# Optimization experiments

Measured on AMD Instinct MI355X. Metric: run time of the kernel, lower is better.

The kernel has to match this reference:

```python
import jax, jax.numpy as jnp
import numpy as np

B, Z, H, T = 256, 512, 1024, 512   # batch, z_size, hidden (conductor==decoder), num_tokens
L, N = 16, 16                      # num_levels, notes_per_bar


def setup_inputs() -> dict:
    key = jax.random.key(0)
    ks = jax.random.split(key, 16)
    s = 0.05  # weight init scale
    rn = lambda k, shp, sc=1.0: sc * jax.random.normal(k, shp, dtype=jnp.float32)
    return {
        "z": rn(ks[0], (B, L * N, 1, Z)),
        "dec_h0": rn(ks[1], (L, B, H)),
        "dec_c0": rn(ks[2], (L, B, H)),
        # linear_in (computed but unused by the original forward)
        "lin_in_W": rn(ks[3], (Z, Z), s), "lin_in_b": rn(ks[4], (Z,), s),
        # conductor LSTM (input Z -> hidden H), PyTorch gate order i,f,g,o
        "cond_Wih": rn(ks[5], (4 * H, Z), s), "cond_Whh": rn(ks[6], (4 * H, H), s),
        "cond_bih": rn(ks[7], (4 * H,), s), "cond_bhh": rn(ks[8], (4 * H,), s),
        # decoder LSTM (input T+H -> hidden H)
        "dec_Wih": rn(ks[9], (4 * H, T + H), s), "dec_Whh": rn(ks[10], (4 * H, H), s),
        "dec_bih": rn(ks[11], (4 * H,), s), "dec_bhh": rn(ks[12], (4 * H,), s),
        # output projection
        "out_W": rn(ks[13], (T, H), s), "out_b": rn(ks[14], (T,), s),
    }


def _lstm_cell(x, h, c, Wih, Whh, b):
    gates = x @ Wih.T + h @ Whh.T + b            # [B, 4H]
    i, f, g, o = jnp.split(gates, 4, axis=-1)
    c = jax.nn.sigmoid(f) * c + jax.nn.sigmoid(i) * jnp.tanh(g)
    h = jax.nn.sigmoid(o) * jnp.tanh(c)
    return h, c


def reference(z, dec_h0, dec_c0, lin_in_W, lin_in_b,
              cond_Wih, cond_Whh, cond_bih, cond_bhh,
              dec_Wih, dec_Whh, dec_bih, dec_bhh, out_W, out_b):
    Bsz = z.shape[0]
    Tt = out_b.shape[0]
    Hh = cond_Whh.shape[1]

    _unused = z @ lin_in_W.T + lin_in_b  # linear_in output is discarded in the source

    cond_b = cond_bih + cond_bhh
    dec_b = dec_bih + dec_bhh

    # conductor consumes z[:, L*level, 0, :] for each level
    z_lv = jnp.transpose(z[:, jnp.arange(L) * L, 0, :], (1, 0, 2))  # [L, B, Z]

    def level_step(carry, xs):
        ch, cc = carry
        zl, dh, dc = xs
        ch, cc = _lstm_cell(zl, ch, cc, cond_Wih, cond_Whh, cond_b)
        emb = ch  # [B, H], fixed conductor embedding for this bar

        def note_step(c2, _):
            note, dh2, dc2 = c2
            inp = jnp.concatenate([emb, note], axis=-1)  # [B, H+T]
            dh2, dc2 = _lstm_cell(inp, dh2, dc2, dec_Wih, dec_Whh, dec_b)
            out = jax.nn.sigmoid(dh2 @ out_W.T + out_b)  # [B, T]
            return (out, dh2, dc2), out

        note0 = jnp.zeros((Bsz, Tt), dtype=z.dtype)
        _, outs = jax.lax.scan(note_step, (note0, dh, dc), None, length=N)  # [N, B, T]
        return (ch, cc), outs

    h0 = jnp.zeros((Bsz, Hh), dtype=z.dtype)
    _, all_outs = jax.lax.scan(level_step, (h0, h0), (z_lv, dec_h0, dec_c0))  # [L, N, B, T]
    notes = jnp.transpose(all_outs, (2, 0, 1, 3)).reshape(Bsz, L * N, Tt)
    return notes
```

## Files before the change

kernel.cpp:

```cpp
#include <hip/hip_runtime.h>

typedef __bf16 bf16;
typedef __attribute__((ext_vector_type(8))) __bf16 bf16x8;
typedef __attribute__((ext_vector_type(4))) float f32x4;
typedef __attribute__((ext_vector_type(4))) unsigned short u16x4;

__device__ __forceinline__ void gload_lds16(const void* g, void* l) {
  __builtin_amdgcn_global_load_lds(
      (const __attribute__((address_space(1))) void*)g,
      (__attribute__((address_space(3))) void*)l, 16, 0, 0);
}

__device__ __forceinline__ float sigmoidf_(float x) { return 1.0f / (1.0f + expf(-x)); }

__device__ __forceinline__ float bf2f(unsigned short u) {
  union { unsigned int i; float f; } v;
  v.i = ((unsigned int)u) << 16;
  return v.f;
}
__device__ __forceinline__ unsigned short f2bfbits(float x) {
  union { bf16 b; unsigned short u; } v;
  v.b = (bf16)x;
  return v.u;
}

#define SB() __builtin_amdgcn_sched_barrier(0)
#define MFMA16(a, b, c) __builtin_amdgcn_mfma_f32_16x16x32_bf16(a, b, c, 0, 0, 0)

template<int MODE>
__global__ __launch_bounds__(512, 2)
void gemm8(const bf16* __restrict__ A, int lda,
           const bf16* __restrict__ Bw, int K,
           bf16* __restrict__ Cb,
           const bf16* __restrict__ X, const float* __restrict__ bias,
           bf16* __restrict__ cst, bf16* __restrict__ hout, int ldh) {
  extern __shared__ __align__(16) char smem_raw[];
  bf16* lsA = (bf16*)smem_raw;
  bf16* lsB = lsA + 4 * 8192;

  const int tid = threadIdx.x;
  const int lane = tid & 63;
  const int wave = tid >> 6;
  const int wm = wave >> 2, wn = wave & 3;

  const int bid = blockIdx.x;
  const int k8 = bid & 7;
  const int l = bid >> 3;
  const int mt = (k8 & 1) * 8 + (l & 7);
  const int nt = (k8 >> 1) * 4 + (l >> 3);
  const int m0 = mt * 256, n0 = nt * 256;

  const int nkt = K >> 5;

  const int srow = tid >> 2;
  const int scol = ((tid & 3) ^ ((srow >> 1) & 3)) * 8;
  const bf16* gAs = A + (size_t)(m0 + srow) * lda + scol;
  const bf16* gBs = Bw + (size_t)(n0 + srow) * K + scol;

  auto stA = [&](int kt) {
    bf16* d = lsA + (kt & 3) * 8192 + tid * 8;
    const bf16* s = gAs + (size_t)kt * 32;
    gload_lds16(s, d);
    gload_lds16(s + (size_t)128 * lda, d + 4096);
  };
  auto stB = [&](int kt) {
    bf16* d = lsB + (kt & 3) * 8192 + tid * 8;
    const bf16* s = gBs + (size_t)kt * 32;
    gload_lds16(s, d);
    gload_lds16(s + (size_t)128 * K, d + 4096);
  };

  const int sw = ((lane & 15) >> 1) & 3;
  const int rslot = ((lane >> 4) ^ sw) * 8;
  const int abase = (wm * 128 + (lane & 15)) * 32 + rslot;
  const int bbase = (wn * 64 + (lane & 15)) * 32 + rslot;

  f32x4 acc[8][4] = {};

  stA(0); stB(0); stA(1); stB(1);
  asm volatile("s_waitcnt vmcnt(4)" ::: "memory");

  for (int t = 0; t < nkt; ++t) {
    SB();
    __builtin_amdgcn_s_barrier();
    SB();
    const bf16* pA = lsA + (t & 3) * 8192;
    const bf16* pB = lsB + (t & 3) * 8192;
    bf16x8 av[8], bv[4];
#pragma unroll
    for (int f = 0; f < 8; ++f) av[f] = *(const bf16x8*)&pA[abase + f * 512];
#pragma unroll
    for (int g = 0; g < 4; ++g) bv[g] = *(const bf16x8*)&pB[bbase + g * 512];
    if (t + 2 < nkt) { stA(t + 2); stB(t + 2); }
    asm volatile("s_waitcnt lgkmcnt(0)" ::: "memory");
    SB();
    __builtin_amdgcn_s_setprio(1);
#pragma unroll
    for (int f = 0; f < 8; ++f)
#pragma unroll
      for (int g = 0; g < 4; ++g)
        acc[f][g] = MFMA16(av[f], bv[g], acc[f][g]);
    __builtin_amdgcn_s_setprio(0);
    if (t + 2 < nkt)      asm volatile("s_waitcnt vmcnt(4)" ::: "memory");
    else if (t + 1 < nkt) asm volatile("s_waitcnt vmcnt(0)" ::: "memory");
  }

  const int jj = lane & 15;
  const int rb = m0 + wm * 128 + ((lane >> 4) << 2);
  const int q = (n0 >> 6) + wn;
  if constexpr (MODE == 0) {
#pragma unroll
    for (int f = 0; f < 8; ++f)
#pragma unroll
      for (int r = 0; r < 4; ++r) {
        u16x4 pk;
        pk[0] = f2bfbits(acc[f][0][r]);
        pk[1] = f2bfbits(acc[f][1][r]);
        pk[2] = f2bfbits(acc[f][2][r]);
        pk[3] = f2bfbits(acc[f][3][r]);
        *(u16x4*)&Cb[(size_t)(rb + f * 16 + r) * 4096 + q * 64 + jj * 4] = pk;
      }
  } else {
    const int j = q * 16 + jj;
    const f32x4 bq = *(const f32x4*)&bias[q * 64 + jj * 4];
#pragma unroll
    for (int f = 0; f < 8; ++f) {
#pragma unroll
      for (int r = 0; r < 4; ++r) {
        const int row = rb + f * 16 + r;
        const u16x4 xv = __builtin_nontemporal_load(
            (const u16x4*)&X[(size_t)row * 4096 + q * 64 + jj * 4]);
        const float gi = acc[f][0][r] + bf2f(xv[0]) + bq[0];
        const float gf = acc[f][1][r] + bf2f(xv[1]) + bq[1];
        const float gg = acc[f][2][r] + bf2f(xv[2]) + bq[2];
        const float go = acc[f][3][r] + bf2f(xv[3]) + bq[3];
        const size_t ci = (size_t)row * 1024 + j;
        const float cold = bf2f(((const unsigned short*)cst)[ci]);
        const float cn = sigmoidf_(gf) * cold + sigmoidf_(gi) * tanhf(gg);
        cst[ci] = (bf16)cn;
        hout[(size_t)row * ldh + j] = (bf16)(sigmoidf_(go) * tanhf(cn));
      }
    }
  }
}

template<int BM, int BN, int WM, int WN, int MODE>
__global__ __launch_bounds__(WM * WN * 64)
void gemm_bt(const bf16* __restrict__ A, int lda,
             const bf16* __restrict__ Bw, int ldb,
             float* __restrict__ C, int ldc, int K,
             const float* __restrict__ outb, float* __restrict__ dout,
             bf16* __restrict__ anote, int nstep) {
  constexpr int BK = 64;
  constexpr int THREADS = WM * WN * 64;
  constexpr int SM = BM / WM, SN = BN / WN;
  constexpr int FM = SM / 16, FN = SN / 16;

  __shared__ __align__(16) bf16 lsA[BM * BK];
  __shared__ __align__(16) bf16 lsB[BN * BK];

  const int tid = threadIdx.x;
  const int lane = tid & 63;
  const int wave = tid >> 6;
  const int wm = wave / WN, wn = wave % WN;

  int mi = blockIdx.y, ni = blockIdx.x;
  if constexpr (MODE == 1) {
    const int flat = blockIdx.y * 8 + blockIdx.x;
    mi = (flat & 7) * 4 + ((flat >> 3) & 3);
    ni = flat >> 5;
  }
  const int m0 = mi * BM;
  const int n0 = ni * BN;

  f32x4 acc[FM][FN] = {};

  const bf16* gA = A + (size_t)m0 * lda;
  const bf16* gB = Bw + (size_t)n0 * ldb;

  for (int k0 = 0; k0 < K; k0 += BK) {
#pragma unroll
    for (int i = 0; i < (BM * 8) / THREADS; ++i) {
      int idx = i * THREADS + tid;
      gload_lds16(gA + (size_t)(idx >> 3) * lda + k0 + (idx & 7) * 8, &lsA[idx * 8]);
    }
#pragma unroll
    for (int i = 0; i < (BN * 8) / THREADS; ++i) {
      int idx = i * THREADS + tid;
      gload_lds16(gB + (size_t)(idx >> 3) * ldb + k0 + (idx & 7) * 8, &lsB[idx * 8]);
    }
    __syncthreads();

#pragma unroll
    for (int kk = 0; kk < BK; kk += 32) {
      bf16x8 av[FM], bv[FN];
#pragma unroll
      for (int i = 0; i < FM; ++i)
        av[i] = *(const bf16x8*)&lsA[(wm * SM + i * 16 + (lane & 15)) * BK + kk + (lane >> 4) * 8];
#pragma unroll
      for (int j = 0; j < FN; ++j)
        bv[j] = *(const bf16x8*)&lsB[(wn * SN + j * 16 + (lane & 15)) * BK + kk + (lane >> 4) * 8];
#pragma unroll
      for (int i = 0; i < FM; ++i)
#pragma unroll
        for (int j = 0; j < FN; ++j)
          acc[i][j] = MFMA16(av[i], bv[j], acc[i][j]);
    }
    __syncthreads();
  }

#pragma unroll
  for (int i = 0; i < FM; ++i) {
#pragma unroll
    for (int j = 0; j < FN; ++j) {
      const int col = n0 + wn * SN + j * 16 + (lane & 15);
      const int rbase = m0 + wm * SM + i * 16 + ((lane >> 4) << 2);
#pragma unroll
      for (int r = 0; r < 4; ++r) {
        const int row = rbase + r;
        float v = acc[i][j][r];
        if constexpr (MODE == 0) {
          C[(size_t)row * ldc + col] = v;
        } else {
          v = sigmoidf_(v + outb[col]);
          const int l = row >> 8, b = row & 255;
          dout[((size_t)(b * 256 + l * 16 + nstep)) * 512 + col] = v;
          anote[(size_t)row * 1536 + col] = (bf16)v;
        }
      }
    }
  }
}

template<int BM, int BJ, int WM, int WJ>
__global__ __launch_bounds__(WM * WJ * 64, 2)
void gemm_cell(const bf16* __restrict__ A, int lda,
               const bf16* __restrict__ Bw,
               const bf16* __restrict__ X,
               const float* __restrict__ bias,
               float* __restrict__ cst,
               bf16* __restrict__ hout, int ldh, int K) {
  constexpr int BK = 64;
  constexpr int THREADS = WM * WJ * 64;
  constexpr int BN = BJ * 64;
  constexpr int SM = BM / WM;
  constexpr int TJ = BJ / WJ;
  constexpr int FM = SM / 16;

  __shared__ __align__(16) bf16 lsA[BM * BK];
  __shared__ __align__(16) bf16 lsB[BN * BK];

  const int tid = threadIdx.x;
  const int lane = tid & 63;
  const int wave = tid >> 6;
  const int wm = wave / WJ, wj = wave % WJ;

  int qbi = blockIdx.x, mi = blockIdx.y;
  if constexpr (BM == 32 && BJ == 2) {
    const int flat = blockIdx.y * 32 + blockIdx.x;
    qbi = (flat & 7) * 4 + ((flat >> 3) & 3);
    mi = flat >> 5;
  }
  const int m0 = mi * BM;
  const int qb = qbi * BJ;

  f32x4 acc[FM][TJ][4] = {};

  const bf16* gA = A + (size_t)m0 * lda;
  const bf16* gB = Bw + (size_t)(qb * 64) * K;

  for (int k0 = 0; k0 < K; k0 += BK) {
#pragma unroll
    for (int i = 0; i < (BM * 8) / THREADS; ++i) {
      int idx = i * THREADS + tid;
      gload_lds16(gA + (size_t)(idx >> 3) * lda + k0 + (idx & 7) * 8, &lsA[idx * 8]);
    }
#pragma unroll
    for (int i = 0; i < (BN * 8) / THREADS; ++i) {
      int idx = i * THREADS + tid;
      gload_lds16(gB + (size_t)(idx >> 3) * K + k0 + (idx & 7) * 8, &lsB[idx * 8]);
    }
    __syncthreads();

#pragma unroll
    for (int kk = 0; kk < BK; kk += 32) {
      bf16x8 av[FM], bv[TJ][4];
#pragma unroll
      for (int i = 0; i < FM; ++i)
        av[i] = *(const bf16x8*)&lsA[(wm * SM + i * 16 + (lane & 15)) * BK + kk + (lane >> 4) * 8];
#pragma unroll
      for (int t = 0; t < TJ; ++t)
#pragma unroll
        for (int g = 0; g < 4; ++g)
          bv[t][g] = *(const bf16x8*)
              &lsB[((wj * TJ + t) * 64 + g * 16 + (lane & 15)) * BK + kk + (lane >> 4) * 8];
#pragma unroll
      for (int i = 0; i < FM; ++i)
#pragma unroll
        for (int t = 0; t < TJ; ++t)
#pragma unroll
          for (int g = 0; g < 4; ++g)
            acc[i][t][g] = MFMA16(av[i], bv[t][g], acc[i][t][g]);
    }
    __syncthreads();
  }

#pragma unroll
  for (int i = 0; i < FM; ++i) {
#pragma unroll
    for (int t = 0; t < TJ; ++t) {
      const int q = qb + wj * TJ + t;
      const int jj = lane & 15;
      const int j = q * 16 + jj;
      const int rbase = m0 + wm * SM + i * 16 + ((lane >> 4) << 2);
      const f32x4 bq = *(const f32x4*)&bias[q * 64 + jj * 4];
#pragma unroll
      for (int r = 0; r < 4; ++r) {
        const int row = rbase + r;
        const u16x4 xv = *(const u16x4*)&X[(size_t)row * 4096 + q * 64 + jj * 4];
        const float gi = acc[i][t][0][r] + bf2f(xv[0]) + bq[0];
        const float gf = acc[i][t][1][r] + bf2f(xv[1]) + bq[1];
        const float gg = acc[i][t][2][r] + bf2f(xv[2]) + bq[2];
        const float go = acc[i][t][3][r] + bf2f(xv[3]) + bq[3];
        const size_t ci = (size_t)row * 1024 + j;
        const float c = sigmoidf_(gf) * cst[ci] + sigmoidf_(gi) * tanhf(gg);
        cst[ci] = c;
        hout[(size_t)row * ldh + j] = (bf16)(sigmoidf_(go) * tanhf(c));
      }
    }
  }
}


__device__ __forceinline__ u16x4 f4_to_bf4(f32x4 v) {
  u16x4 o;
  o[0] = f2bfbits(v[0]); o[1] = f2bfbits(v[1]);
  o[2] = f2bfbits(v[2]); o[3] = f2bfbits(v[3]);
  return o;
}

__device__ __forceinline__ int p_src_row(int n) {
  int q = n >> 6, gate = (n >> 4) & 3, jj = n & 15;
  return gate * 1024 + q * 16 + jj;
}

__global__ void conv_f32_bf16_4(const float* __restrict__ src, bf16* __restrict__ dst) {
  int idx = (blockIdx.x * 256 + threadIdx.x) * 4;
  *(u16x4*)&dst[idx] = f4_to_bf4(*(const f32x4*)&src[idx]);
}

__global__ void pack_w_dec(const float* __restrict__ wih, const float* __restrict__ whh,
                           bf16* __restrict__ dst) {
  int idx = (blockIdx.x * 256 + threadIdx.x) * 4;
  int n = idx / 1536, c = idx - n * 1536;
  int r = p_src_row(n);
  const float* s = (c < 512) ? &wih[(size_t)r * 1536 + 1024 + c]
                             : &whh[(size_t)r * 1024 + (c - 512)];
  *(u16x4*)&dst[idx] = f4_to_bf4(*(const f32x4*)s);
}

__global__ void pack_w_emb(const float* __restrict__ wih, bf16* __restrict__ dst) {
  int idx = (blockIdx.x * 256 + threadIdx.x) * 4;
  int n = idx >> 10, c = idx & 1023;
  *(u16x4*)&dst[idx] = f4_to_bf4(*(const f32x4*)&wih[(size_t)p_src_row(n) * 1536 + c]);
}

__global__ void pack_w_perm(const float* __restrict__ src, bf16* __restrict__ dst, int Kw) {
  int idx = (blockIdx.x * 256 + threadIdx.x) * 4;
  int n = idx / Kw, c = idx - n * Kw;
  *(u16x4*)&dst[idx] = f4_to_bf4(*(const f32x4*)&src[(size_t)p_src_row(n) * Kw + c]);
}

__global__ void pack_bias2(const float* __restrict__ dbih, const float* __restrict__ dbhh,
                           float* __restrict__ ddst,
                           const float* __restrict__ cbih, const float* __restrict__ cbhh,
                           float* __restrict__ cdst) {
  int n = blockIdx.x * 256 + threadIdx.x;
  int q = n >> 6, jj = (n >> 2) & 15, g = n & 3;
  int r = g * 1024 + q * 16 + jj;
  ddst[n] = dbih[r] + dbhh[r];
  cdst[n] = cbih[r] + cbhh[r];
}

__global__ void pack_zb(const float* __restrict__ z, bf16* __restrict__ dst) {
  int idx = (blockIdx.x * 256 + threadIdx.x) * 4;
  int m = idx >> 9, k = idx & 511;
  int l = m >> 8, b = m & 255;
  *(u16x4*)&dst[idx] =
      f4_to_bf4(*(const f32x4*)&z[((size_t)b * 256 + 16 * l) * 512 + k]);
}

__global__ void init_cond(float* __restrict__ cc, bf16* __restrict__ hz0) {
  int idx = (blockIdx.x * 256 + threadIdx.x) * 4;
  *(f32x4*)&cc[idx] = f32x4{0.f, 0.f, 0.f, 0.f};
  *(u16x4*)&hz0[idx] = u16x4{0, 0, 0, 0};
}

__global__ void init_state(const float* __restrict__ h0, const float* __restrict__ c0,
                           bf16* __restrict__ Abuf, bf16* __restrict__ cdec) {
  int idx = (blockIdx.x * 256 + threadIdx.x) * 4;
  int m = idx / 1536, c = idx - m * 1536;
  if (c < 512) {
    *(u16x4*)&Abuf[idx] = u16x4{0, 0, 0, 0};
  } else {
    int j = c - 512;
    size_t s = (size_t)m * 1024 + j;
    *(u16x4*)&Abuf[idx] = f4_to_bf4(*(const f32x4*)&h0[s]);
    *(u16x4*)&cdec[s] = f4_to_bf4(*(const f32x4*)&c0[s]);
  }
}

extern "C" void kernel_launch(void* const* d_in, const int* in_sizes, int n_in,
                              void* d_out, int out_size, void* d_ws, size_t ws_size,
                              hipStream_t stream) {
  const float* z        = (const float*)d_in[0];
  const float* dec_h0   = (const float*)d_in[1];
  const float* dec_c0   = (const float*)d_in[2];
  const float* cond_Wih = (const float*)d_in[5];
  const float* cond_Whh = (const float*)d_in[6];
  const float* cond_bih = (const float*)d_in[7];
  const float* cond_bhh = (const float*)d_in[8];
  const float* dec_Wih  = (const float*)d_in[9];
  const float* dec_Whh  = (const float*)d_in[10];
  const float* dec_bih  = (const float*)d_in[11];
  const float* dec_bhh  = (const float*)d_in[12];
  const float* out_W    = (const float*)d_in[13];
  const float* out_b    = (const float*)d_in[14];
  float* out = (float*)d_out;

  char* ws = (char*)d_ws;
  size_t off = 0;
  auto alloc = [&](size_t bytes) {
    void* p = ws + off;
    off += (bytes + 255) & ~(size_t)255;
    return p;
  };
  bf16* E     = (bf16*)alloc(4096ull * 4096 * 2);
  bf16* Xz    = (bf16*)alloc(4096ull * 4096 * 2);
  bf16* cdec  = (bf16*)alloc(4096ull * 1024 * 2);
  bf16* Ab0   = (bf16*)alloc(4096ull * 1536 * 2);
  bf16* Ab1   = (bf16*)alloc(4096ull * 1536 * 2);
  bf16* Wd    = (bf16*)alloc(4096ull * 1536 * 2);
  bf16* We    = (bf16*)alloc(4096ull * 1024 * 2);
  bf16* Wcih  = (bf16*)alloc(4096ull * 512 * 2);
  bf16* Wchh  = (bf16*)alloc(4096ull * 1024 * 2);
  bf16* Wo    = (bf16*)alloc(512ull * 1024 * 2);
  float* cc   = (float*)alloc(256ull * 1024 * 4);
  bf16* emb   = (bf16*)alloc(4096ull * 1024 * 2);
  bf16* Zb    = (bf16*)alloc(4096ull * 512 * 2);
  bf16* hz0   = (bf16*)alloc(256ull * 1024 * 2);
  float* bdP  = (float*)alloc(4096ull * 4);
  float* bcP  = (float*)alloc(4096ull * 4);

  dim3 b256(256);

  hipFuncSetAttribute(reinterpret_cast<const void*>(&gemm8<0>),
                      hipFuncAttributeMaxDynamicSharedMemorySize, 131072);
  hipFuncSetAttribute(reinterpret_cast<const void*>(&gemm8<1>),
                      hipFuncAttributeMaxDynamicSharedMemorySize, 131072);

  pack_w_perm<<<4096 * 512 / 1024, b256, 0, stream>>>(cond_Wih, Wcih, 512);
  pack_w_perm<<<4096 * 1024 / 1024, b256, 0, stream>>>(cond_Whh, Wchh, 1024);
  conv_f32_bf16_4<<<512 * 1024 / 1024, b256, 0, stream>>>(out_W, Wo);
  pack_w_dec<<<4096 * 1536 / 1024, b256, 0, stream>>>(dec_Wih, dec_Whh, Wd);
  pack_w_emb<<<4096 * 1024 / 1024, b256, 0, stream>>>(dec_Wih, We);
  pack_bias2<<<16, b256, 0, stream>>>(dec_bih, dec_bhh, bdP, cond_bih, cond_bhh, bcP);
  pack_zb<<<4096 * 512 / 1024, b256, 0, stream>>>(z, Zb);
  init_cond<<<256 * 1024 / 1024, b256, 0, stream>>>(cc, hz0);
  init_state<<<4096 * 1536 / 1024, b256, 0, stream>>>(dec_h0, dec_c0, Ab0, cdec);

  gemm8<0><<<256, 512, 131072, stream>>>(Zb, 512, Wcih, 512, Xz,
                                         nullptr, nullptr, nullptr, nullptr, 0);

  for (int l = 0; l < 16; ++l) {
    const bf16* hprev = (l == 0) ? hz0 : (emb + (size_t)(l - 1) * 256 * 1024);
    gemm_cell<32, 2, 2, 2><<<dim3(32, 8), dim3(256), 0, stream>>>(
        hprev, 1024, Wchh, Xz + (size_t)l * 256 * 4096, bcP,
        cc, emb + (size_t)l * 256 * 1024, 1024, 1024);
  }

  gemm8<0><<<256, 512, 131072, stream>>>(emb, 1024, We, 1024, E,
                                         nullptr, nullptr, nullptr, nullptr, 0);

  for (int n = 0; n < 16; ++n) {
    bf16* Sc = (n & 1) ? Ab1 : Ab0;
    bf16* Sn = (n & 1) ? Ab0 : Ab1;
    gemm8<1><<<256, 512, 131072, stream>>>(Sc, 1536, Wd, 1536, nullptr,
                                           E, bdP, cdec, Sn + 512, 1536);
    gemm_bt<128, 64, 2, 2, 1><<<dim3(8, 32), dim3(256), 0, stream>>>(
        Sn + 512, 1536, Wo, 1024, nullptr, 0, 1024, out_b, out, Sn, n);
  }
}
```

Baseline: 1.797 ms.

## Stagger wave groups in GEMM so MFMA overlaps LDS reads, remap tile order

Splits the eight waves of the GEMM block into two groups that run out of phase. The first group loads LDS fragments and then runs MFMAs on them in the same iteration. The second group runs MFMAs on the previous iteration's fragments before loading the current ones, and drains the last tile after the loop. The aim is for one group's LDS reads and global prefetch to overlap the other group's matrix math on the same SIMD. The block-to-tile mapping is also changed to a different XCD-interleaved order. The risks are extra register pressure from fragments kept live across iterations, and possible changes in L2 locality from the new tile order.

```diff
diff --git a/kernel.cpp b/kernel.cpp
--- a/kernel.cpp
+++ b/kernel.cpp
@@ -42,13 +42,11 @@
   const int lane = tid & 63;
   const int wave = tid >> 6;
   const int wm = wave >> 2, wn = wave & 3;
+  const int grp = wm;
 
   const int bid = blockIdx.x;
-  const int k8 = bid & 7;
-  const int l = bid >> 3;
-  const int mt = (k8 & 1) * 8 + (l & 7);
-  const int nt = (k8 >> 1) * 4 + (l >> 3);
-  const int m0 = mt * 256, n0 = nt * 256;
+  const int wgid = (bid & 7) * 32 + (bid >> 3);
+  const int m0 = (wgid & 15) * 256, n0 = (wgid >> 4) * 256;
 
   const int nkt = K >> 5;
 
@@ -76,6 +74,7 @@
   const int bbase = (wn * 64 + (lane & 15)) * 32 + rslot;
 
   f32x4 acc[8][4] = {};
+  bf16x8 av[8], bv[4];
 
   stA(0); stB(0); stA(1); stB(1);
   asm volatile("s_waitcnt vmcnt(4)" ::: "memory");
@@ -86,23 +85,54 @@
     SB();
     const bf16* pA = lsA + (t & 3) * 8192;
     const bf16* pB = lsB + (t & 3) * 8192;
-    bf16x8 av[8], bv[4];
-#pragma unroll
-    for (int f = 0; f < 8; ++f) av[f] = *(const bf16x8*)&pA[abase + f * 512];
-#pragma unroll
-    for (int g = 0; g < 4; ++g) bv[g] = *(const bf16x8*)&pB[bbase + g * 512];
-    if (t + 2 < nkt) { stA(t + 2); stB(t + 2); }
+
+    if (grp == 0) {
+#pragma unroll
+      for (int f = 0; f < 8; ++f) av[f] = *(const bf16x8*)&pA[abase + f * 512];
+#pragma unroll
+      for (int g = 0; g < 4; ++g) bv[g] = *(const bf16x8*)&pB[bbase + g * 512];
+      if (t + 2 < nkt) { stA(t + 2); stB(t + 2); }
+      asm volatile("s_waitcnt lgkmcnt(0)" ::: "memory");
+      SB();
+      __builtin_amdgcn_s_setprio(1);
+#pragma unroll
+      for (int f = 0; f < 8; ++f)
+#pragma unroll
+        for (int g = 0; g < 4; ++g)
+          acc[f][g] = MFMA16(av[f], bv[g], acc[f][g]);
+      __builtin_amdgcn_s_setprio(0);
+    } else {
+      asm volatile("s_waitcnt lgkmcnt(0)" ::: "memory");
+      SB();
+      if (t > 0) {
+        __builtin_amdgcn_s_setprio(1);
+#pragma unroll
+        for (int f = 0; f < 8; ++f)
+#pragma unroll
+          for (int g = 0; g < 4; ++g)
+            acc[f][g] = MFMA16(av[f], bv[g], acc[f][g]);
+        __builtin_amdgcn_s_setprio(0);
+      }
+      SB();
+#pragma unroll
+      for (int f = 0; f < 8; ++f) av[f] = *(const bf16x8*)&pA[abase + f * 512];
+#pragma unroll
+      for (int g = 0; g < 4; ++g) bv[g] = *(const bf16x8*)&pB[bbase + g * 512];
+      if (t + 2 < nkt) { stA(t + 2); stB(t + 2); }
+    }
+
+    if (t + 2 < nkt)      asm volatile("s_waitcnt vmcnt(4)" ::: "memory");
+    else if (t + 1 < nkt) asm volatile("s_waitcnt vmcnt(0)" ::: "memory");
+  }
+
+  if (grp == 1) {
     asm volatile("s_waitcnt lgkmcnt(0)" ::: "memory");
     SB();
-    __builtin_amdgcn_s_setprio(1);
 #pragma unroll
     for (int f = 0; f < 8; ++f)
 #pragma unroll
       for (int g = 0; g < 4; ++g)
         acc[f][g] = MFMA16(av[f], bv[g], acc[f][g]);
-    __builtin_amdgcn_s_setprio(0);
-    if (t + 2 < nkt)      asm volatile("s_waitcnt vmcnt(4)" ::: "memory");
-    else if (t + 1 < nkt) asm volatile("s_waitcnt vmcnt(0)" ::: "memory");
   }
 
   const int jj = lane & 15;
```

Measured after the change: 1.806 ms. About the same (+0.5%).

## Replace per-step kernel launches with persistent cooperative kernels using grid sync

Applied to the files above, without the earlier changes.

Folds the 16-step conductor LSTM loop and the 16-step decoder loop (cell GEMM plus output projection) into two persistent cooperative kernels. Grid-wide syncs now separate the dependent steps instead of separate kernel launches. This targets launch overhead and the tail gaps between the roughly 48 small dependent kernels. In exchange, the output projection now runs with a 512-thread block shape inside the decoder kernel. Grid sync cost and cooperative-launch occupancy limits (256 blocks of 512 threads with 128KB LDS) may hurt throughput.

```diff
diff --git a/kernel.cpp b/kernel.cpp
--- a/kernel.cpp
+++ b/kernel.cpp
@@ -1,4 +1,7 @@
 #include <hip/hip_runtime.h>
+#include <hip/hip_cooperative_groups.h>
+
+namespace cg = cooperative_groups;
 
 typedef __bf16 bf16;
 typedef __attribute__((ext_vector_type(8))) __bf16 bf16x8;
@@ -31,9 +34,7 @@
 __global__ __launch_bounds__(512, 2)
 void gemm8(const bf16* __restrict__ A, int lda,
            const bf16* __restrict__ Bw, int K,
-           bf16* __restrict__ Cb,
-           const bf16* __restrict__ X, const float* __restrict__ bias,
-           bf16* __restrict__ cst, bf16* __restrict__ hout, int ldh) {
+           bf16* __restrict__ Cb) {
   extern __shared__ __align__(16) char smem_raw[];
   bf16* lsA = (bf16*)smem_raw;
   bf16* lsB = lsA + 4 * 8192;
@@ -44,11 +45,8 @@
   const int wm = wave >> 2, wn = wave & 3;
 
   const int bid = blockIdx.x;
-  const int k8 = bid & 7;
-  const int l = bid >> 3;
-  const int mt = (k8 & 1) * 8 + (l & 7);
-  const int nt = (k8 >> 1) * 4 + (l >> 3);
-  const int m0 = mt * 256, n0 = nt * 256;
+  const int wgid = (bid & 7) * 32 + (bid >> 3);
+  const int m0 = (wgid & 15) * 256, n0 = (wgid >> 4) * 256;
 
   const int nkt = K >> 5;
 
@@ -108,199 +106,164 @@
   const int jj = lane & 15;
   const int rb = m0 + wm * 128 + ((lane >> 4) << 2);
   const int q = (n0 >> 6) + wn;
-  if constexpr (MODE == 0) {
-#pragma unroll
-    for (int f = 0; f < 8; ++f)
-#pragma unroll
-      for (int r = 0; r < 4; ++r) {
-        u16x4 pk;
-        pk[0] = f2bfbits(acc[f][0][r]);
-        pk[1] = f2bfbits(acc[f][1][r]);
-        pk[2] = f2bfbits(acc[f][2][r]);
-        pk[3] = f2bfbits(acc[f][3][r]);
-        *(u16x4*)&Cb[(size_t)(rb + f * 16 + r) * 4096 + q * 64 + jj * 4] = pk;
-      }
-  } else {
-    const int j = q * 16 + jj;
-    const f32x4 bq = *(const f32x4*)&bias[q * 64 + jj * 4];
-#pragma unroll
-    for (int f = 0; f < 8; ++f) {
-#pragma unroll
-      for (int r = 0; r < 4; ++r) {
-        const int row = rb + f * 16 + r;
-        const u16x4 xv = __builtin_nontemporal_load(
-            (const u16x4*)&X[(size_t)row * 4096 + q * 64 + jj * 4]);
-        const float gi = acc[f][0][r] + bf2f(xv[0]) + bq[0];
-        const float gf = acc[f][1][r] + bf2f(xv[1]) + bq[1];
-        const float gg = acc[f][2][r] + bf2f(xv[2]) + bq[2];
-        const float go = acc[f][3][r] + bf2f(xv[3]) + bq[3];
-        const size_t ci = (size_t)row * 1024 + j;
-        const float cold = bf2f(((const unsigned short*)cst)[ci]);
-        const float cn = sigmoidf_(gf) * cold + sigmoidf_(gi) * tanhf(gg);
-        cst[ci] = (bf16)cn;
-        hout[(size_t)row * ldh + j] = (bf16)(sigmoidf_(go) * tanhf(cn));
-      }
-    }
-  }
-}
-
-template<int BM, int BN, int WM, int WN, int MODE>
-__global__ __launch_bounds__(WM * WN * 64)
-void gemm_bt(const bf16* __restrict__ A, int lda,
-             const bf16* __restrict__ Bw, int ldb,
-             float* __restrict__ C, int ldc, int K,
-             const float* __restrict__ outb, float* __restrict__ dout,
-             bf16* __restrict__ anote, int nstep) {
-  constexpr int BK = 64;
-  constexpr int THREADS = WM * WN * 64;
-  constexpr int SM = BM / WM, SN = BN / WN;
-  constexpr int FM = SM / 16, FN = SN / 16;
-
-  __shared__ __align__(16) bf16 lsA[BM * BK];
-  __shared__ __align__(16) bf16 lsB[BN * BK];
+#pragma unroll
+  for (int f = 0; f < 8; ++f)
+#pragma unroll
+    for (int r = 0; r < 4; ++r) {
+      u16x4 pk;
+      pk[0] = f2bfbits(acc[f][0][r]);
+      pk[1] = f2bfbits(acc[f][1][r]);
+      pk[2] = f2bfbits(acc[f][2][r]);
+      pk[3] = f2bfbits(acc[f][3][r]);
+      *(u16x4*)&Cb[(size_t)(rb + f * 16 + r) * 4096 + q * 64 + jj * 4] = pk;
+    }
+}
+
+__device__ __forceinline__ void dec_step_body(
+    char* smem_raw, const bf16* __restrict__ Sc, const bf16* __restrict__ Wd,
+    const bf16* __restrict__ E, const float* __restrict__ bias,
+    bf16* __restrict__ cst, bf16* __restrict__ hout) {
+  bf16* lsA = (bf16*)smem_raw;
+  bf16* lsB = lsA + 4 * 8192;
 
   const int tid = threadIdx.x;
   const int lane = tid & 63;
   const int wave = tid >> 6;
-  const int wm = wave / WN, wn = wave % WN;
-
-  int mi = blockIdx.y, ni = blockIdx.x;
-  if constexpr (MODE == 1) {
-    const int flat = blockIdx.y * 8 + blockIdx.x;
-    mi = (flat & 7) * 4 + ((flat >> 3) & 3);
-    ni = flat >> 5;
-  }
-  const int m0 = mi * BM;
-  const int n0 = ni * BN;
-
-  f32x4 acc[FM][FN] = {};
-
-  const bf16* gA = A + (size_t)m0 * lda;
-  const bf16* gB = Bw + (size_t)n0 * ldb;
-
-  for (int k0 = 0; k0 < K; k0 += BK) {
-#pragma unroll
-    for (int i = 0; i < (BM * 8) / THREADS; ++i) {
-      int idx = i * THREADS + tid;
-      gload_lds16(gA + (size_t)(idx >> 3) * lda + k0 + (idx & 7) * 8, &lsA[idx * 8]);
-    }
-#pragma unroll
-    for (int i = 0; i < (BN * 8) / THREADS; ++i) {
-      int idx = i * THREADS + tid;
-      gload_lds16(gB + (size_t)(idx >> 3) * ldb + k0 + (idx & 7) * 8, &lsB[idx * 8]);
-    }
-    __syncthreads();
-
-#pragma unroll
-    for (int kk = 0; kk < BK; kk += 32) {
-      bf16x8 av[FM], bv[FN];
-#pragma unroll
-      for (int i = 0; i < FM; ++i)
-        av[i] = *(const bf16x8*)&lsA[(wm * SM + i * 16 + (lane & 15)) * BK + kk + (lane >> 4) * 8];
-#pragma unroll
-      for (int j = 0; j < FN; ++j)
-        bv[j] = *(const bf16x8*)&lsB[(wn * SN + j * 16 + (lane & 15)) * BK + kk + (lane >> 4) * 8];
-#pragma unroll
-      for (int i = 0; i < FM; ++i)
-#pragma unroll
-        for (int j = 0; j < FN; ++j)
-          acc[i][j] = MFMA16(av[i], bv[j], acc[i][j]);
-    }
-    __syncthreads();
-  }
-
-#pragma unroll
-  for (int i = 0; i < FM; ++i) {
-#pragma unroll
-    for (int j = 0; j < FN; ++j) {
-      const int col = n0 + wn * SN + j * 16 + (lane & 15);
-      const int rbase = m0 + wm * SM + i * 16 + ((lane >> 4) << 2);
-#pragma unroll
-      for (int r = 0; r < 4; ++r) {
-        const int row = rbase + r;
-        float v = acc[i][j][r];
-        if constexpr (MODE == 0) {
-          C[(size_t)row * ldc + col] = v;
-        } else {
-          v = sigmoidf_(v + outb[col]);
-          const int l = row >> 8, b = row & 255;
-          dout[((size_t)(b * 256 + l * 16 + nstep)) * 512 + col] = v;
-          anote[(size_t)row * 1536 + col] = (bf16)v;
-        }
-      }
-    }
-  }
-}
-
-template<int BM, int BJ, int WM, int WJ>
-__global__ __launch_bounds__(WM * WJ * 64, 2)
-void gemm_cell(const bf16* __restrict__ A, int lda,
-               const bf16* __restrict__ Bw,
-               const bf16* __restrict__ X,
-               const float* __restrict__ bias,
-               float* __restrict__ cst,
-               bf16* __restrict__ hout, int ldh, int K) {
-  constexpr int BK = 64;
-  constexpr int THREADS = WM * WJ * 64;
-  constexpr int BN = BJ * 64;
-  constexpr int SM = BM / WM;
-  constexpr int TJ = BJ / WJ;
-  constexpr int FM = SM / 16;
-
-  __shared__ __align__(16) bf16 lsA[BM * BK];
-  __shared__ __align__(16) bf16 lsB[BN * BK];
+  const int wm = wave >> 2, wn = wave & 3;
+
+  const int bid = blockIdx.x;
+  const int wgid = (bid & 7) * 32 + (bid >> 3);
+  const int m0 = (wgid & 15) * 256, n0 = (wgid >> 4) * 256;
+
+  constexpr int K = 1536, lda = 1536, ldh = 1536;
+  constexpr int nkt = K >> 5;
+
+  const int srow = tid >> 2;
+  const int scol = ((tid & 3) ^ ((srow >> 1) & 3)) * 8;
+  const bf16* gAs = Sc + (size_t)(m0 + srow) * lda + scol;
+  const bf16* gBs = Wd + (size_t)(n0 + srow) * K + scol;
+
+  auto stA = [&](int kt) {
+    bf16* d = lsA + (kt & 3) * 8192 + tid * 8;
+    const bf16* s = gAs + (size_t)kt * 32;
+    gload_lds16(s, d);
+    gload_lds16(s + (size_t)128 * lda, d + 4096);
+  };
+  auto stB = [&](int kt) {
+    bf16* d = lsB + (kt & 3) * 8192 + tid * 8;
+    const bf16* s = gBs + (size_t)kt * 32;
+    gload_lds16(s, d);
+    gload_lds16(s + (size_t)128 * K, d + 4096);
+  };
+
+  const int sw = ((lane & 15) >> 1) & 3;
+  const int rslot = ((lane >> 4) ^ sw) * 8;
+  const int abase = (wm * 128 + (lane & 15)) * 32 + rslot;
+  const int bbase = (wn * 64 + (lane & 15)) * 32 + rslot;
+
+  f32x4 acc[8][4] = {};
+
+  stA(0); stB(0); stA(1); stB(1);
+  asm volatile("s_waitcnt vmcnt(4)" ::: "memory");
+
+  for (int t = 0; t < nkt; ++t) {
+    SB();
+    __builtin_amdgcn_s_barrier();
+    SB();
+    const bf16* pA = lsA + (t & 3) * 8192;
+    const bf16* pB = lsB + (t & 3) * 8192;
+    bf16x8 av[8], bv[4];
+#pragma unroll
+    for (int f = 0; f < 8; ++f) av[f] = *(const bf16x8*)&pA[abase + f * 512];
+#pragma unroll
+    for (int g = 0; g < 4; ++g) bv[g] = *(const bf16x8*)&pB[bbase + g * 512];
+    if (t + 2 < nkt) { stA(t + 2); stB(t + 2); }
+    asm volatile("s_waitcnt lgkmcnt(0)" ::: "memory");
+    SB();
+    __builtin_amdgcn_s_setprio(1);
+#pragma unroll
+    for (int f = 0; f < 8; ++f)
+#pragma unroll
+      for (int g = 0; g < 4; ++g)
+        acc[f][g] = MFMA16(av[f], bv[g], acc[f][g]);
+    __builtin_amdgcn_s_setprio(0);
+    if (t + 2 < nkt)      asm volatile("s_waitcnt vmcnt(4)" ::: "memory");
+    else if (t + 1 < nkt) asm volatile("s_waitcnt vmcnt(0)" ::: "memory");
+  }
+
+  const int jj = lane & 15;
+  const int rb = m0 + wm * 128 + ((lane >> 4) << 2);
+  const int q = (n0 >> 6) + wn;
+  const int j = q * 16 + jj;
+  const f32x4 bq = *(const f32x4*)&bias[q * 64 + jj * 4];
+#pragma unroll
+  for (int f = 0; f < 8; ++f) {
+#pragma unroll
+    for (int r = 0; r < 4; ++r) {
+      const int row = rb + f * 16 + r;
+      const u16x4 xv = __builtin_nontemporal_load(
+          (const u16x4*)&E[(size_t)row * 4096 + q * 64 + jj * 4]);
+      const float gi = acc[f][0][r] + bf2f(xv[0]) + bq[0];
+      const float gf = acc[f][1][r] + bf2f(xv[1]) + bq[1];
+      const float gg = acc[f][2][r] + bf2f(xv[2]) + bq[2];
+      const float go = acc[f][3][r] + bf2f(xv[3]) + bq[3];
+      const size_t ci = (size_t)row * 1024 + j;
+      const float cold = bf2f(((const unsigned short*)cst)[ci]);
+      const float cn = sigmoidf_(gf) * cold + sigmoidf_(gi) * tanhf(gg);
+      cst[ci] = (bf16)cn;
+      hout[(size_t)row * ldh + j] = (bf16)(sigmoidf_(go) * tanhf(cn));
+    }
+  }
+}
+
+__device__ __forceinline__ void outproj_body(
+    char* smem_raw, const bf16* __restrict__ A, const bf16* __restrict__ Bw,
+    const float* __restrict__ outb, float* __restrict__ dout,
+    bf16* __restrict__ anote, int nstep) {
+  constexpr int BM = 128, BN = 64, BK = 64;
+  constexpr int SM = 32, SN = 32, FM = 2, FN = 2;
+  constexpr int lda = 1536, ldb = 1024, K = 1024;
+  bf16* lsA = (bf16*)smem_raw;
+  bf16* lsB = lsA + BM * BK;
 
   const int tid = threadIdx.x;
   const int lane = tid & 63;
   const int wave = tid >> 6;
-  const int wm = wave / WJ, wj = wave % WJ;
-
-  int qbi = blockIdx.x, mi = blockIdx.y;
-  if constexpr (BM == 32 && BJ == 2) {
-    const int flat = blockIdx.y * 32 + blockIdx.x;
-    qbi = (flat & 7) * 4 + ((flat >> 3) & 3);
-    mi = flat >> 5;
-  }
-  const int m0 = mi * BM;
-  const int qb = qbi * BJ;
-
-  f32x4 acc[FM][TJ][4] = {};
+  const int wm = wave >> 1, wn = wave & 1;
+
+  const int bid = blockIdx.x;
+  const int mi = (bid & 7) * 4 + ((bid >> 3) & 3);
+  const int ni = bid >> 5;
+  const int m0 = mi * BM, n0 = ni * BN;
+
+  f32x4 acc[FM][FN] = {};
 
   const bf16* gA = A + (size_t)m0 * lda;
-  const bf16* gB = Bw + (size_t)(qb * 64) * K;
+  const bf16* gB = Bw + (size_t)n0 * ldb;
 
   for (int k0 = 0; k0 < K; k0 += BK) {
 #pragma unroll
-    for (int i = 0; i < (BM * 8) / THREADS; ++i) {
-      int idx = i * THREADS + tid;
+    for (int i = 0; i < 2; ++i) {
+      int idx = i * 512 + tid;
       gload_lds16(gA + (size_t)(idx >> 3) * lda + k0 + (idx & 7) * 8, &lsA[idx * 8]);
     }
-#pragma unroll
-    for (int i = 0; i < (BN * 8) / THREADS; ++i) {
-      int idx = i * THREADS + tid;
-      gload_lds16(gB + (size_t)(idx >> 3) * K + k0 + (idx & 7) * 8, &lsB[idx * 8]);
-    }
+    gload_lds16(gB + (size_t)(tid >> 3) * ldb + k0 + (tid & 7) * 8, &lsB[tid * 8]);
     __syncthreads();
 
 #pragma unroll
     for (int kk = 0; kk < BK; kk += 32) {
-      bf16x8 av[FM], bv[TJ][4];
+      bf16x8 av[FM], bv[FN];
 #pragma unroll
       for (int i = 0; i < FM; ++i)
         av[i] = *(const bf16x8*)&lsA[(wm * SM + i * 16 + (lane & 15)) * BK + kk + (lane >> 4) * 8];
 #pragma unroll
-      for (int t = 0; t < TJ; ++t)
-#pragma unroll
-        for (int g = 0; g < 4; ++g)
-          bv[t][g] = *(const bf16x8*)
-              &lsB[((wj * TJ + t) * 64 + g * 16 + (lane & 15)) * BK + kk + (lane >> 4) * 8];
+      for (int jf = 0; jf < FN; ++jf)
+        bv[jf] = *(const bf16x8*)&lsB[(wn * SN + jf * 16 + (lane & 15)) * BK + kk + (lane >> 4) * 8];
 #pragma unroll
       for (int i = 0; i < FM; ++i)
 #pragma unroll
-        for (int t = 0; t < TJ; ++t)
-#pragma unroll
-          for (int g = 0; g < 4; ++g)
-            acc[i][t][g] = MFMA16(av[i], bv[t][g], acc[i][t][g]);
+        for (int jf = 0; jf < FN; ++jf)
+          acc[i][jf] = MFMA16(av[i], bv[jf], acc[i][jf]);
     }
     __syncthreads();
   }
@@ -308,26 +271,118 @@
 #pragma unroll
   for (int i = 0; i < FM; ++i) {
 #pragma unroll
-    for (int t = 0; t < TJ; ++t) {
-      const int q = qb + wj * TJ + t;
-      const int jj = lane & 15;
-      const int j = q * 16 + jj;
+    for (int jf = 0; jf < FN; ++jf) {
+      const int col = n0 + wn * SN + jf * 16 + (lane & 15);
       const int rbase = m0 + wm * SM + i * 16 + ((lane >> 4) << 2);
-      const f32x4 bq = *(const f32x4*)&bias[q * 64 + jj * 4];
 #pragma unroll
       for (int r = 0; r < 4; ++r) {
         const int row = rbase + r;
-        const u16x4 xv = *(const u16x4*)&X[(size_t)row * 4096 + q * 64 + jj * 4];
-        const float gi = acc[i][t][0][r] + bf2f(xv[0]) + bq[0];
-        const float gf = acc[i][t][1][r] + bf2f(xv[1]) + bq[1];
-        const float gg = acc[i][t][2][r] + bf2f(xv[2]) + bq[2];
-        const float go = acc[i][t][3][r] + bf2f(xv[3]) + bq[3];
-        const size_t ci = (size_t)row * 1024 + j;
-        const float c = sigmoidf_(gf) * cst[ci] + sigmoidf_(gi) * tanhf(gg);
-        cst[ci] = c;
-        hout[(size_t)row * ldh + j] = (bf16)(sigmoidf_(go) * tanhf(c));
+        float v = sigmoidf_(acc[i][jf][r] + outb[col]);
+        const int l = row >> 8, b = row & 255;
+        dout[((size_t)(b * 256 + l * 16 + nstep)) * 512 + col] = v;
+        anote[(size_t)row * 1536 + col] = (bf16)v;
       }
     }
+  }
+}
+
+__global__ __launch_bounds__(512, 2)
+void dec_loop(const bf16* __restrict__ Wd, const bf16* __restrict__ E,
+              const float* __restrict__ bdP, bf16* __restrict__ cdec,
+              bf16* __restrict__ Ab0, bf16* __restrict__ Ab1,
+              const bf16* __restrict__ Wo, const float* __restrict__ outb,
+              float* __restrict__ out) {
+  extern __shared__ __align__(16) char smem_raw[];
+  cg::grid_group grid = cg::this_grid();
+  for (int n = 0; n < 16; ++n) {
+    bf16* Sc = (n & 1) ? Ab1 : Ab0;
+    bf16* Sn = (n & 1) ? Ab0 : Ab1;
+    dec_step_body(smem_raw, Sc, Wd, E, bdP, cdec, Sn + 512);
+    grid.sync();
+    outproj_body(smem_raw, Sn + 512, Wo, outb, out, Sn, n);
+    grid.sync();
+  }
+}
+
+__device__ __forceinline__ void cond_cell_body(
+    const bf16* __restrict__ A, const bf16* __restrict__ Bw,
+    const bf16* __restrict__ X, const float* __restrict__ bias,
+    float* __restrict__ cst, bf16* __restrict__ hout) {
+  constexpr int BK = 64, K = 1024;
+  __shared__ __align__(16) bf16 lsA[32 * BK];
+  __shared__ __align__(16) bf16 lsB[128 * BK];
+
+  const int tid = threadIdx.x;
+  const int lane = tid & 63;
+  const int wave = tid >> 6;
+  const int wm = wave >> 1, wj = wave & 1;
+
+  const int flat = blockIdx.x;
+  const int qbi = (flat & 7) * 4 + ((flat >> 3) & 3);
+  const int mi = flat >> 5;
+  const int m0 = mi * 32;
+  const int qb = qbi * 2;
+
+  f32x4 acc[1][4] = {};
+
+  const bf16* gA = A + (size_t)m0 * 1024;
+  const bf16* gB = Bw + (size_t)(qb * 64) * K;
+
+  for (int k0 = 0; k0 < K; k0 += BK) {
+    {
+      int idx = tid;
+      gload_lds16(gA + (size_t)(idx >> 3) * 1024 + k0 + (idx & 7) * 8, &lsA[idx * 8]);
+    }
+#pragma unroll
+    for (int i = 0; i < 4; ++i) {
+      int idx = i * 256 + tid;
+      gload_lds16(gB + (size_t)(idx >> 3) * K + k0 + (idx & 7) * 8, &lsB[idx * 8]);
+    }
+    __syncthreads();
+
+#pragma unroll
+    for (int kk = 0; kk < BK; kk += 32) {
+      bf16x8 av = *(const bf16x8*)&lsA[(wm * 16 + (lane & 15)) * BK + kk + (lane >> 4) * 8];
+#pragma unroll
+      for (int g = 0; g < 4; ++g) {
+        bf16x8 bv = *(const bf16x8*)
+            &lsB[((wj * 1) * 64 + g * 16 + (lane & 15)) * BK + kk + (lane >> 4) * 8];
+        acc[0][g] = MFMA16(av, bv, acc[0][g]);
+      }
+    }
+    __syncthreads();
+  }
+
+  const int q = qb + wj;
+  const int jj = lane & 15;
+  const int j = q * 16 + jj;
+  const int rbase = m0 + wm * 16 + ((lane >> 4) << 2);
+  const f32x4 bq = *(const f32x4*)&bias[q * 64 + jj * 4];
+#pragma unroll
+  for (int r = 0; r < 4; ++r) {
+    const int row = rbase + r;
+    const u16x4 xv = *(const u16x4*)&X[(size_t)row * 4096 + q * 64 + jj * 4];
+    const float gi = acc[0][0][r] + bf2f(xv[0]) + bq[0];
+    const float gf = acc[0][1][r] + bf2f(xv[1]) + bq[1];
+    const float gg = acc[0][2][r] + bf2f(xv[2]) + bq[2];
+    const float go = acc[0][3][r] + bf2f(xv[3]) + bq[3];
+    const size_t ci = (size_t)row * 1024 + j;
+    const float c = sigmoidf_(gf) * cst[ci] + sigmoidf_(gi) * tanhf(gg);
+    cst[ci] = c;
+    hout[(size_t)row * 1024 + j] = (bf16)(sigmoidf_(go) * tanhf(c));
+  }
+}
+
+__global__ __launch_bounds__(256, 2)
+void cond_chain(const bf16* __restrict__ hz0, const bf16* __restrict__ Wchh,
+                const bf16* __restrict__ Xz, const float* __restrict__ bias,
+                float* __restrict__ cc, bf16* __restrict__ emb) {
+  cg::grid_group grid = cg::this_grid();
+  for (int l = 0; l < 16; ++l) {
+    const bf16* A = (l == 0) ? hz0 : emb + (size_t)(l - 1) * 262144;
+    cond_cell_body(A, Wchh, Xz + (size_t)l * 1048576, bias, cc,
+                   emb + (size_t)l * 262144);
+    grid.sync();
   }
 }
 
@@ -456,7 +511,7 @@
 
   hipFuncSetAttribute(reinterpret_cast<const void*>(&gemm8<0>),
                       hipFuncAttributeMaxDynamicSharedMemorySize, 131072);
-  hipFuncSetAttribute(reinterpret_cast<const void*>(&gemm8<1>),
+  hipFuncSetAttribute(reinterpret_cast<const void*>(&dec_loop),
                       hipFuncAttributeMaxDynamicSharedMemorySize, 131072);
 
   pack_w_perm<<<4096 * 512 / 1024, b256, 0, stream>>>(cond_Wih, Wcih, 512);
@@ -469,25 +524,22 @@
   init_cond<<<256 * 1024 / 1024, b256, 0, stream>>>(cc, hz0);
   init_state<<<4096 * 1536 / 1024, b256, 0, stream>>>(dec_h0, dec_c0, Ab0, cdec);
 
-  gemm8<0><<<256, 512, 131072, stream>>>(Zb, 512, Wcih, 512, Xz,
-                                         nullptr, nullptr, nullptr, nullptr, 0);
-
-  for (int l = 0; l < 16; ++l) {
-    const bf16* hprev = (l == 0) ? hz0 : (emb + (size_t)(l - 1) * 256 * 1024);
-    gemm_cell<32, 2, 2, 2><<<dim3(32, 8), dim3(256), 0, stream>>>(
-        hprev, 1024, Wchh, Xz + (size_t)l * 256 * 4096, bcP,
-        cc, emb + (size_t)l * 256 * 1024, 1024, 1024);
-  }
-
-  gemm8<0><<<256, 512, 131072, stream>>>(emb, 1024, We, 1024, E,
-                                         nullptr, nullptr, nullptr, nullptr, 0);
-
-  for (int n = 0; n < 16; ++n) {
-    bf16* Sc = (n & 1) ? Ab1 : Ab0;
-    bf16* Sn = (n & 1) ? Ab0 : Ab1;
-    gemm8<1><<<256, 512, 131072, stream>>>(Sc, 1536, Wd, 1536, nullptr,
-                                           E, bdP, cdec, Sn + 512, 1536);
-    gemm_bt<128, 64, 2, 2, 1><<<dim3(8, 32), dim3(256), 0, stream>>>(
-        Sn + 512, 1536, Wo, 1024, nullptr, 0, 1024, out_b, out, Sn, n);
-  }
-}
+  gemm8<0><<<256, 512, 131072, stream>>>(Zb, 512, Wcih, 512, Xz);
+
+  {
+    void* args[] = {(void*)&hz0, (void*)&Wchh, (void*)&Xz, (void*)&bcP,
+                    (void*)&cc, (void*)&emb};
+    hipLaunchCooperativeKernel(reinterpret_cast<void*>(&cond_chain),
+                               dim3(256), dim3(256), args, 0, stream);
+  }
+
+  gemm8<0><<<256, 512, 131072, stream>>>(emb, 1024, We, 1024, E);
+
+  {
+    void* args[] = {(void*)&Wd, (void*)&E, (void*)&bdP, (void*)&cdec,
+                    (void*)&Ab0, (void*)&Ab1, (void*)&Wo, (void*)&out_b,
+                    (void*)&out};
+    hipLaunchCooperativeKernel(reinterpret_cast<void*>(&dec_loop),
+                               dim3(256), dim3(512), args, 131072, stream);
+  }
+}
```

Result: slower. 3.626 ms (+101.8%).
